# Performance work log

Hardware: AMD Instinct MI355X
Metric: run time of the kernel (lower is better)

Reference implementation:

```python
import jax, jax.numpy as jnp
import numpy as np

N, E = 50000, 800000
IN_DIM, NH = 256, 64          # in_dim, num_hidden
HID = 2 * NH                  # per-head out of GAT layers = num_hidden*2 = 128
HEADS, C = 2, 32              # heads[0]=heads[1]=2, final head=1, num_classes=32
NEG = 0.2                     # leaky relu negative slope


def _gat(h, W, al, ar, b, src, dst, heads, out, identity_res=False, res_W=None, act=None):
    # DGL-style GATConv: linear -> per-head attn logits -> edge softmax over dst -> scatter sum
    n = h.shape[0]
    feat = (h @ W).reshape(n, heads, out)              # [N, H, D]
    el = (feat * al).sum(-1)                           # [N, H]
    er = (feat * ar).sum(-1)                           # [N, H]
    e = el[src] + er[dst]                              # [E, H]
    e = jnp.where(e > 0, e, NEG * e)                   # leaky relu
    emax = jax.ops.segment_max(e, dst, num_segments=n)
    ex = jnp.exp(e - emax[dst])
    den = jax.ops.segment_sum(ex, dst, num_segments=n)
    alpha = ex / den[dst]                              # edge softmax per dst
    msg = feat[src] * alpha[..., None]                 # [E, H, D]
    rst = jax.ops.segment_sum(msg, dst, num_segments=n)  # [N, H, D]
    if identity_res:
        rst = rst + h.reshape(n, heads, out)
    elif res_W is not None:
        rst = rst + (h @ res_W).reshape(n, heads, out)
    rst = rst + b.reshape(1, heads, out)
    return act(rst) if act is not None else rst


def setup_inputs() -> dict:
    key = jax.random.key(0)
    ks = jax.random.split(key, 24)
    g = lambda i, shp, s: jax.random.normal(ks[i], shp, jnp.float32) * s
    d = {
        'inputs': g(0, (N, IN_DIM), 1.0),
        'z': g(1, (NH,), 1.0),
        'src': jax.random.randint(ks[2], (E,), 0, N, jnp.int32),
        'dst': jax.random.randint(ks[3], (E,), 0, N, jnp.int32),
        # x_to_h
        'Wx': g(4, (IN_DIM, NH), 0.06), 'bx': jnp.zeros((NH,), jnp.float32),
        # GAT layer 0: in 2*NH=128 -> heads=2, out=128
        'W0': g(5, (HID, HEADS * HID), 0.09), 'al0': g(6, (HEADS, HID), 0.09),
        'ar0': g(7, (HEADS, HID), 0.09), 'b0': jnp.zeros((HEADS * HID,), jnp.float32),
        # GAT layer 1: in 256 -> heads=2, out=128 (identity residual)
        'W1': g(8, (HEADS * HID, HEADS * HID), 0.06), 'al1': g(9, (HEADS, HID), 0.09),
        'ar1': g(10, (HEADS, HID), 0.09), 'b1': jnp.zeros((HEADS * HID,), jnp.float32),
        # final GAT: in 256 -> 1 head, out=num_classes=32, linear residual
        'Wf': g(11, (HEADS * HID, C), 0.06), 'alf': g(12, (1, C), 0.18),
        'arf': g(13, (1, C), 0.18), 'bf': jnp.zeros((C,), jnp.float32),
        'resWf': g(14, (HEADS * HID, C), 0.06),
    }
    return d


def reference(inputs, z, src, dst, Wx, bx, W0, al0, ar0, b0, W1, al1, ar1, b1, Wf, alf, arf, bf, resWf):
    n = inputs.shape[0]
    h = jax.nn.relu(inputs @ Wx + bx)                          # [N, NH]
    h = jnp.concatenate([h, jnp.broadcast_to(z, (n, z.shape[0]))], axis=1)  # [N, 2*NH]
    h = h / (jnp.linalg.norm(h, axis=1, keepdims=True) + 1e-6)
    h = _gat(h, W0, al0, ar0, b0, src, dst, HEADS, HID, act=jax.nn.elu).reshape(n, -1)
    h = _gat(h, W1, al1, ar1, b1, src, dst, HEADS, HID, identity_res=True, act=jax.nn.elu).reshape(n, -1)
    logits = _gat(h, Wf, alf, arf, bf, src, dst, 1, C, res_W=resWf).mean(1)  # [N, C]
    return logits
```

## Files before the change

### kernel.cpp

```cpp
#include <hip/hip_runtime.h>
#include <hip/hip_bf16.h>
#include <math.h>

#define N_NODES 50000
#define N_EDGES 800000
#define NEG 0.2f

typedef __attribute__((ext_vector_type(4))) float f32x4;
typedef __attribute__((ext_vector_type(8))) short bf16x8;

__device__ __forceinline__ float bf2f(ushort u) {
    union { uint i; float f; } t; t.i = ((uint)u) << 16; return t.f;
}
__device__ __forceinline__ ushort f2bf(float f) {
    union { float f; uint i; } t; t.f = f;
    uint i = t.i;
    uint r = (i + 0x7FFFu + ((i >> 16) & 1u)) >> 16;
    return (ushort)r;
}
__device__ __forceinline__ uint cvtpk(float lo, float hi) {
    uint r;
    asm("v_cvt_pk_bf16_f32 %0, %1, %2" : "=v"(r) : "v"(lo), "v"(hi));
    return r;
}

__device__ __forceinline__ void gload16(const ushort* src, ushort* ldst) {
    __builtin_amdgcn_global_load_lds(
        (const __attribute__((address_space(1))) uint32_t*)src,
        (__attribute__((address_space(3))) uint32_t*)ldst, 16, 0, 0);
}

__global__ void k_fillp(const int* __restrict__ src, const int* __restrict__ dst,
                        int* __restrict__ cnt, int* __restrict__ esrc, int E) {
    int e = blockIdx.x * 256 + threadIdx.x;
    if (e < E) {
        int d = dst[e];
        int p = atomicAdd(&cnt[d], 1);
        if (p < 64) esrc[((size_t)d << 6) + p] = src[e];
    }
}

__global__ void k_prep2(const float* __restrict__ Wx, const float* __restrict__ W0,
                        const float* __restrict__ W1, const float* __restrict__ Wf,
                        const float* __restrict__ rWf, const float* __restrict__ z,
                        ushort* __restrict__ BtX, ushort* __restrict__ Bt0,
                        ushort* __restrict__ Bt1, ushort* __restrict__ BtF,
                        float* __restrict__ zW0, int* __restrict__ cnt) {
    int i = blockIdx.x * 256 + threadIdx.x;
    const int base3 = 131072 + 256;
    if (i < 16384) {
        int n = i >> 8, k = i & 255;
        BtX[i] = f2bf(Wx[k * 64 + n]);
    } else if (i < 49152) {
        int t = i - 16384;
        int n = t >> 7, k = t & 127;
        Bt0[t] = f2bf(W0[k * 256 + n]);
    } else if (i < 114688) {
        int t = i - 49152;
        int n = t >> 8, k = t & 255;
        Bt1[t] = f2bf(W1[k * 256 + n]);
    } else if (i < 131072) {
        int t = i - 114688;
        int n = t >> 8, k = t & 255;
        float v = (n < 32) ? Wf[k * 32 + n] : rWf[k * 32 + (n - 32)];
        BtF[t] = f2bf(v);
    } else if (i < base3) {
        int c = i - 131072;
        float s = 0.f;
        for (int k = 0; k < 64; ++k) s += z[k] * W0[(64 + k) * 256 + c];
        zW0[c] = s;
    } else if (i < base3 + N_NODES) {
        cnt[i - base3] = 0;
    }
}

__global__ __launch_bounds__(256) void k_gemmA(
    const float* __restrict__ Ax, const ushort* __restrict__ BtX,
    const ushort* __restrict__ Bt0, const float* __restrict__ bx,
    const float* __restrict__ zv, const float* __restrict__ zW0,
    const float* __restrict__ alv, const float* __restrict__ arv,
    ushort* __restrict__ feat, float* __restrict__ elv, float* __restrict__ erv, int M)
{
    __shared__ ushort As1[128 * 64];
    __shared__ ushort Bs1[64 * 64];
    __shared__ ushort As2[128 * 64];
    __shared__ ushort Bs2[256 * 64];
    __shared__ float  invRow[128];

    const int tid = threadIdx.x;
    const int bm = blockIdx.x * 128;
    const int lane = tid & 63;
    const int w = tid >> 6;
    const int fr = lane & 15;
    const int kg = lane >> 4;
    const int rl = lane >> 3;
    const int bl = lane & 7;

    #pragma unroll
    for (int i = w; i < 32; i += 4) {
        int r = i * 8 + rl;
        int cb = bl ^ (r & 7);
        gload16(Bt0 + (size_t)r * 128 + cb * 8, &Bs2[i * 512]);
    }

    f32x4 acc1[2][4];
    #pragma unroll
    for (int m = 0; m < 2; ++m)
        #pragma unroll
        for (int n = 0; n < 4; ++n) acc1[m][n] = (f32x4){0.f, 0.f, 0.f, 0.f};

    const int ar_ = tid >> 1;
    const int ab_ = (tid & 1) * 4;
    int agr = bm + ar_; if (agr >= M) agr = 0;
    const float* ap0 = Ax + (size_t)agr * 256 + ab_ * 8;

    for (int k0 = 0; k0 < 256; k0 += 64) {
        {
            const float* ap = ap0 + k0;
            #pragma unroll
            for (int b = 0; b < 4; ++b) {
                float4 v0 = *(const float4*)(ap + b * 8);
                float4 v1 = *(const float4*)(ap + b * 8 + 4);
                uint4 pk;
                pk.x = cvtpk(v0.x, v0.y);
                pk.y = cvtpk(v0.z, v0.w);
                pk.z = cvtpk(v1.x, v1.y);
                pk.w = cvtpk(v1.z, v1.w);
                int p = (ab_ + b) ^ (ar_ & 7);
                *(uint4*)&As1[ar_ * 64 + p * 8] = pk;
            }
        }
        #pragma unroll
        for (int i = w; i < 8; i += 4) {
            int r = i * 8 + rl;
            int cb = bl ^ (r & 7);
            gload16(BtX + (size_t)r * 256 + k0 + cb * 8, &Bs1[i * 512]);
        }
        __syncthreads();
        #pragma unroll
        for (int s = 0; s < 2; ++s) {
            bf16x8 a[2], b[4];
            #pragma unroll
            for (int m = 0; m < 2; ++m) {
                int row = w * 32 + m * 16 + fr;
                int blk = (s * 4 + kg) ^ (fr & 7);
                a[m] = *(const bf16x8*)&As1[row * 64 + blk * 8];
            }
            #pragma unroll
            for (int n = 0; n < 4; ++n) {
                int row = n * 16 + fr;
                int blk = (s * 4 + kg) ^ (fr & 7);
                b[n] = *(const bf16x8*)&Bs1[row * 64 + blk * 8];
            }
            #pragma unroll
            for (int m = 0; m < 2; ++m)
                #pragma unroll
                for (int n = 0; n < 4; ++n)
                    acc1[m][n] = __builtin_amdgcn_mfma_f32_16x16x32_bf16(a[m], b[n], acc1[m][n], 0, 0, 0);
        }
        __syncthreads();
    }

    {
        float zl = zv[lane];
        float zq = zl * zl;
        #pragma unroll
        for (int off = 32; off > 0; off >>= 1) zq += __shfl_xor(zq, off, 64);
        #pragma unroll
        for (int m = 0; m < 2; ++m) {
            #pragma unroll
            for (int j = 0; j < 4; ++j) {
                int row = w * 32 + m * 16 + kg * 4 + j;
                float v[4]; float ss = 0.f;
                #pragma unroll
                for (int n = 0; n < 4; ++n) {
                    float o = acc1[m][n][j] + bx[n * 16 + fr];
                    o = fmaxf(o, 0.f);
                    v[n] = o; ss += o * o;
                }
                #pragma unroll
                for (int off = 8; off > 0; off >>= 1) ss += __shfl_xor(ss, off, 64);
                float inv = 1.f / (sqrtf(ss + zq) + 1e-6f);
                if (fr == 0) invRow[row] = inv;
                #pragma unroll
                for (int n = 0; n < 4; ++n) {
                    int b = n * 2 + (fr >> 3);
                    int p = b ^ (row & 7);
                    As2[row * 64 + p * 8 + (fr & 7)] = f2bf(v[n] * inv);
                }
            }
        }
    }
    __syncthreads();

    const int wr2 = w >> 1, wc2 = w & 1;
    f32x4 acc2[4][8];
    #pragma unroll
    for (int m = 0; m < 4; ++m)
        #pragma unroll
        for (int n = 0; n < 8; ++n) acc2[m][n] = (f32x4){0.f, 0.f, 0.f, 0.f};
    #pragma unroll
    for (int s = 0; s < 2; ++s) {
        bf16x8 a[4], b[8];
        #pragma unroll
        for (int m = 0; m < 4; ++m) {
            int row = wr2 * 64 + m * 16 + fr;
            int blk = (s * 4 + kg) ^ (fr & 7);
            a[m] = *(const bf16x8*)&As2[row * 64 + blk * 8];
        }
        #pragma unroll
        for (int n = 0; n < 8; ++n) {
            int row = wc2 * 128 + n * 16 + fr;
            int blk = (s * 4 + kg) ^ (fr & 7);
            b[n] = *(const bf16x8*)&Bs2[row * 64 + blk * 8];
        }
        #pragma unroll
        for (int m = 0; m < 4; ++m)
            #pragma unroll
            for (int n = 0; n < 8; ++n)
                acc2[m][n] = __builtin_amdgcn_mfma_f32_16x16x32_bf16(a[m], b[n], acc2[m][n], 0, 0, 0);
    }

    #pragma unroll
    for (int m = 0; m < 4; ++m) {
        #pragma unroll
        for (int j = 0; j < 4; ++j) {
            int lrow = wr2 * 64 + m * 16 + kg * 4 + j;
            int row = bm + lrow;
            float invR = invRow[lrow];
            float pe = 0.f, pr = 0.f;
            if (row < M) {
                #pragma unroll
                for (int n = 0; n < 8; ++n) {
                    int col = wc2 * 128 + n * 16 + fr;
                    float o = acc2[m][n][j] + invR * zW0[col];
                    feat[(size_t)row * 256 + col] = f2bf(o);
                    pe += o * alv[col];
                    pr += o * arv[col];
                }
            }
            #pragma unroll
            for (int off = 8; off > 0; off >>= 1) {
                pe += __shfl_xor(pe, off, 64);
                pr += __shfl_xor(pr, off, 64);
            }
            if (row < M && fr == 0) {
                elv[(size_t)row * 2 + wc2] = pe;
                erv[(size_t)row * 2 + wc2] = pr;
            }
        }
    }
}

__global__ __launch_bounds__(256) void k_gemmB(
    const ushort* __restrict__ A, const ushort* __restrict__ Bt,
    ushort* __restrict__ feat, const float* __restrict__ alv, const float* __restrict__ arv,
    float* __restrict__ elv, float* __restrict__ erv, int M)
{
    __shared__ ushort As[128 * 64];
    __shared__ ushort Bs[256 * 64];

    const int tid = threadIdx.x;
    const int bm = blockIdx.x * 128;
    const int lane = tid & 63;
    const int w = tid >> 6;
    const int wr = w >> 1, wc = w & 1;
    const int fr = lane & 15;
    const int kg = lane >> 4;
    const int rl = lane >> 3;
    const int bl = lane & 7;

    f32x4 acc[4][8];
    #pragma unroll
    for (int m = 0; m < 4; ++m)
        #pragma unroll
        for (int n = 0; n < 8; ++n) acc[m][n] = (f32x4){0.f, 0.f, 0.f, 0.f};

    for (int k0 = 0; k0 < 256; k0 += 64) {
        #pragma unroll
        for (int i = w; i < 16; i += 4) {
            int r = i * 8 + rl;
            int cb = bl ^ (r & 7);
            int gr = bm + r;
            if (gr >= M) gr = 0;
            gload16(A + (size_t)gr * 256 + k0 + cb * 8, &As[i * 512]);
        }
        #pragma unroll
        for (int i = w; i < 32; i += 4) {
            int r = i * 8 + rl;
            int cb = bl ^ (r & 7);
            gload16(Bt + (size_t)r * 256 + k0 + cb * 8, &Bs[i * 512]);
        }
        __syncthreads();
        #pragma unroll
        for (int s = 0; s < 2; ++s) {
            bf16x8 a[4], b[8];
            #pragma unroll
            for (int m = 0; m < 4; ++m) {
                int row = wr * 64 + m * 16 + fr;
                int blk = (s * 4 + kg) ^ (fr & 7);
                a[m] = *(const bf16x8*)&As[row * 64 + blk * 8];
            }
            #pragma unroll
            for (int n = 0; n < 8; ++n) {
                int row = wc * 128 + n * 16 + fr;
                int blk = (s * 4 + kg) ^ (fr & 7);
                b[n] = *(const bf16x8*)&Bs[row * 64 + blk * 8];
            }
            #pragma unroll
            for (int m = 0; m < 4; ++m)
                #pragma unroll
                for (int n = 0; n < 8; ++n)
                    acc[m][n] = __builtin_amdgcn_mfma_f32_16x16x32_bf16(a[m], b[n], acc[m][n], 0, 0, 0);
        }
        __syncthreads();
    }

    #pragma unroll
    for (int m = 0; m < 4; ++m) {
        #pragma unroll
        for (int j = 0; j < 4; ++j) {
            int row = bm + wr * 64 + m * 16 + kg * 4 + j;
            float pe = 0.f, pr = 0.f;
            if (row < M) {
                #pragma unroll
                for (int n = 0; n < 8; ++n) {
                    int col = wc * 128 + n * 16 + fr;
                    float o = acc[m][n][j];
                    feat[(size_t)row * 256 + col] = f2bf(o);
                    pe += o * alv[col];
                    pr += o * arv[col];
                }
            }
            #pragma unroll
            for (int off = 8; off > 0; off >>= 1) {
                pe += __shfl_xor(pe, off, 64);
                pr += __shfl_xor(pr, off, 64);
            }
            if (row < M && fr == 0) {
                elv[(size_t)row * 2 + wc] = pe;
                erv[(size_t)row * 2 + wc] = pr;
            }
        }
    }
}

__global__ __launch_bounds__(256) void k_gemmC(
    const ushort* __restrict__ A, const ushort* __restrict__ Bt,
    ushort* __restrict__ pkb, float* __restrict__ C2,
    const float* __restrict__ alv, const float* __restrict__ arv,
    float* __restrict__ elv, float* __restrict__ erv, int M)
{
    __shared__ ushort As[128 * 64];
    __shared__ ushort Bs[64 * 64];

    const int tid = threadIdx.x;
    const int bm = blockIdx.x * 128;
    const int lane = tid & 63;
    const int w = tid >> 6;
    const int fr = lane & 15;
    const int kg = lane >> 4;
    const int rl = lane >> 3;
    const int bl = lane & 7;

    f32x4 acc[2][4];
    #pragma unroll
    for (int m = 0; m < 2; ++m)
        #pragma unroll
        for (int n = 0; n < 4; ++n) acc[m][n] = (f32x4){0.f, 0.f, 0.f, 0.f};

    for (int k0 = 0; k0 < 256; k0 += 64) {
        #pragma unroll
        for (int i = w; i < 16; i += 4) {
            int r = i * 8 + rl;
            int cb = bl ^ (r & 7);
            int gr = bm + r;
            if (gr >= M) gr = 0;
            gload16(A + (size_t)gr * 256 + k0 + cb * 8, &As[i * 512]);
        }
        #pragma unroll
        for (int i = w; i < 8; i += 4) {
            int r = i * 8 + rl;
            int cb = bl ^ (r & 7);
            gload16(Bt + (size_t)r * 256 + k0 + cb * 8, &Bs[i * 512]);
        }
        __syncthreads();
        #pragma unroll
        for (int s = 0; s < 2; ++s) {
            bf16x8 a[2], b[4];
            #pragma unroll
            for (int m = 0; m < 2; ++m) {
                int row = w * 32 + m * 16 + fr;
                int blk = (s * 4 + kg) ^ (fr & 7);
                a[m] = *(const bf16x8*)&As[row * 64 + blk * 8];
            }
            #pragma unroll
            for (int n = 0; n < 4; ++n) {
                int row = n * 16 + fr;
                int blk = (s * 4 + kg) ^ (fr & 7);
                b[n] = *(const bf16x8*)&Bs[row * 64 + blk * 8];
            }
            #pragma unroll
            for (int m = 0; m < 2; ++m)
                #pragma unroll
                for (int n = 0; n < 4; ++n)
                    acc[m][n] = __builtin_amdgcn_mfma_f32_16x16x32_bf16(a[m], b[n], acc[m][n], 0, 0, 0);
        }
        __syncthreads();
    }

    #pragma unroll
    for (int m = 0; m < 2; ++m) {
        #pragma unroll
        for (int j = 0; j < 4; ++j) {
            int row = bm + w * 32 + m * 16 + kg * 4 + j;
            float pe = 0.f, pr = 0.f;
            if (row < M) {
                #pragma unroll
                for (int n = 0; n < 4; ++n) {
                    int col = n * 16 + fr;
                    float o = acc[m][n][j];
                    pkb[(size_t)row * 64 + col] = f2bf(o);
                    if (n >= 2) {
                        C2[(size_t)row * 32 + (col - 32)] = o;
                    } else {
                        pe += o * alv[col];
                        pr += o * arv[col];
                    }
                }
            }
            #pragma unroll
            for (int off = 8; off > 0; off >>= 1) {
                pe += __shfl_xor(pe, off, 64);
                pr += __shfl_xor(pr, off, 64);
            }
            if (row < M && fr == 0) { elv[row] = pe; erv[row] = pr; }
        }
    }
}

template<int RES>
__global__ __launch_bounds__(256) void k_edge256(
    const ushort* __restrict__ feat, const float* __restrict__ el, const float* __restrict__ er,
    const float* __restrict__ bias, const int* __restrict__ cnt, const int* __restrict__ esrc,
    ushort* __restrict__ outp, const ushort* __restrict__ resid, int n)
{
    __shared__ int2 swb[4][2][32];
    int wid = (blockIdx.x * blockDim.x + threadIdx.x) >> 6;
    int lane = threadIdx.x & 63;
    int w = threadIdx.x >> 6;
    if (wid >= n) return;
    int m = lane & 31;
    int head = lane >> 5;
    int deg = cnt[wid]; if (deg > 64) deg = 64;
    int rs = wid << 6, re = rs + deg;
    float ern = er[((size_t)wid << 1) + head];
    const char* featc = (const char*)feat;
    uint loff = (uint)lane << 3;

    float den[4] = {0.f, 0.f, 0.f, 0.f};
    f32x4 av[4];
    #pragma unroll
    for (int u = 0; u < 4; ++u) av[u] = (f32x4){0.f, 0.f, 0.f, 0.f};

    for (int c = rs; c < re; c += 32) {
        int nj = re - c; if (nj > 32) nj = 32;
        if (m < nj) {
            int s = esrc[c + m];
            float x = el[((uint)s << 1) + head] + ern;
            x = (x > 0.f) ? x : NEG * x;
            float wv = __expf(fminf(x, 60.f));
            int2 t; t.x = s; t.y = __float_as_int(wv);
            swb[w][head][m] = t;
        }
        int j = 0;
        for (; j + 3 < nj; j += 4) {
            #pragma unroll
            for (int u = 0; u < 4; ++u) {
                int2 p = swb[w][head][j + u];
                float wU = __int_as_float(p.y);
                ushort4 vU = *(const ushort4*)(featc + (((uint)p.x << 9) | loff));
                den[u] += wU;
                av[u].x += wU * bf2f(vU.x);
                av[u].y += wU * bf2f(vU.y);
                av[u].z += wU * bf2f(vU.z);
                av[u].w += wU * bf2f(vU.w);
            }
        }
        for (; j < nj; ++j) {
            int2 p = swb[w][head][j];
            float wU = __int_as_float(p.y);
            ushort4 vU = *(const ushort4*)(featc + (((uint)p.x << 9) | loff));
            den[0] += wU;
            av[0].x += wU * bf2f(vU.x);
            av[0].y += wU * bf2f(vU.y);
            av[0].z += wU * bf2f(vU.z);
            av[0].w += wU * bf2f(vU.w);
        }
    }
    float denT = (den[0] + den[1]) + (den[2] + den[3]);
    float ax = (av[0].x + av[1].x) + (av[2].x + av[3].x);
    float ay = (av[0].y + av[1].y) + (av[2].y + av[3].y);
    float az = (av[0].z + av[1].z) + (av[2].z + av[3].z);
    float aw = (av[0].w + av[1].w) + (av[2].w + av[3].w);
    float inv = (deg > 0) ? 1.f / denT : 0.f;

    int c0i = lane * 4;
    float4 bv = *(const float4*)(bias + c0i);
    float rx = 0.f, ry = 0.f, rz = 0.f, rw = 0.f;
    if (RES) {
        ushort4 rv = ((const ushort4*)resid)[(size_t)wid * 64 + lane];
        rx = bf2f(rv.x); ry = bf2f(rv.y); rz = bf2f(rv.z); rw = bf2f(rv.w);
    }
    float ox = ax * inv + bv.x + rx;
    float oy = ay * inv + bv.y + ry;
    float oz = az * inv + bv.z + rz;
    float ow = aw * inv + bv.w + rw;
    ox = (ox > 0.f) ? ox : expm1f(ox);
    oy = (oy > 0.f) ? oy : expm1f(oy);
    oz = (oz > 0.f) ? oz : expm1f(oz);
    ow = (ow > 0.f) ? ow : expm1f(ow);
    ushort4 o;
    o.x = f2bf(ox); o.y = f2bf(oy); o.z = f2bf(oz); o.w = f2bf(ow);
    ((ushort4*)outp)[(size_t)wid * 64 + lane] = o;
}

__global__ __launch_bounds__(256) void k_edgef(
    const ushort* __restrict__ pkb, const float* __restrict__ residf,
    const float* __restrict__ elf, const float* __restrict__ erf,
    const float* __restrict__ bfv, const int* __restrict__ cnt, const int* __restrict__ esrc,
    float* __restrict__ outp, int n)
{
    __shared__ int2 swf[16][16];
    int t = blockIdx.x * 256 + threadIdx.x;
    int node = t >> 4;
    int m = t & 15;
    int nb = threadIdx.x >> 4;
    if (node >= n) return;
    int deg = cnt[node]; if (deg > 64) deg = 64;
    int rs = node << 6, re = rs + deg;
    float ern = erf[node];
    const char* pc = (const char*)pkb;
    uint moff = (uint)m << 2;

    float den[4] = {0.f, 0.f, 0.f, 0.f};
    float a0[4] = {0.f, 0.f, 0.f, 0.f};
    float a1[4] = {0.f, 0.f, 0.f, 0.f};

    for (int c = rs; c < re; c += 16) {
        int nj = re - c; if (nj > 16) nj = 16;
        if (m < nj) {
            int s = esrc[c + m];
            float x = elf[s] + ern;
            x = (x > 0.f) ? x : NEG * x;
            float wv = __expf(fminf(x, 60.f));
            int2 tt; tt.x = s; tt.y = __float_as_int(wv);
            swf[nb][m] = tt;
        }
        int j = 0;
        for (; j + 3 < nj; j += 4) {
            #pragma unroll
            for (int u = 0; u < 4; ++u) {
                int2 p = swf[nb][j + u];
                float wU = __int_as_float(p.y);
                ushort2 vU = *(const ushort2*)(pc + (((uint)p.x << 7) | moff));
                den[u] += wU;
                a0[u] += wU * bf2f(vU.x);
                a1[u] += wU * bf2f(vU.y);
            }
        }
        for (; j < nj; ++j) {
            int2 p = swf[nb][j];
            float wU = __int_as_float(p.y);
            ushort2 vU = *(const ushort2*)(pc + (((uint)p.x << 7) | moff));
            den[0] += wU;
            a0[0] += wU * bf2f(vU.x);
            a1[0] += wU * bf2f(vU.y);
        }
    }
    float dT = (den[0] + den[1]) + (den[2] + den[3]);
    float A0 = (a0[0] + a0[1]) + (a0[2] + a0[3]);
    float A1 = (a1[0] + a1[1]) + (a1[2] + a1[3]);
    float inv = (deg > 0) ? 1.f / dT : 0.f;

    float2 rv = *(const float2*)(residf + (size_t)node * 32 + 2 * m);
    float2 bv = *(const float2*)(bfv + 2 * m);
    float2 o;
    o.x = A0 * inv + rv.x + bv.x;
    o.y = A1 * inv + rv.y + bv.y;
    *(float2*)(outp + (size_t)node * 32 + 2 * m) = o;
}

extern "C" void kernel_launch(void* const* d_in, const int* in_sizes, int n_in,
                              void* d_out, int out_size, void* d_ws, size_t ws_size,
                              hipStream_t stream) {
    const float* inputs = (const float*)d_in[0];
    const float* z      = (const float*)d_in[1];
    const int*   src    = (const int*)d_in[2];
    const int*   dst    = (const int*)d_in[3];
    const float* Wx  = (const float*)d_in[4];
    const float* bx  = (const float*)d_in[5];
    const float* W0  = (const float*)d_in[6];
    const float* al0 = (const float*)d_in[7];
    const float* ar0 = (const float*)d_in[8];
    const float* b0  = (const float*)d_in[9];
    const float* W1  = (const float*)d_in[10];
    const float* al1 = (const float*)d_in[11];
    const float* ar1 = (const float*)d_in[12];
    const float* b1  = (const float*)d_in[13];
    const float* Wf  = (const float*)d_in[14];
    const float* alf = (const float*)d_in[15];
    const float* arf = (const float*)d_in[16];
    const float* bf  = (const float*)d_in[17];
    const float* rWf = (const float*)d_in[18];
    float* out = (float*)d_out;

    const int N = N_NODES, E = N_EDGES;

    char* w = (char*)d_ws;
    auto alloc = [&](size_t bytes) -> char* {
        char* p = w;
        w += (bytes + 255) & ~(size_t)255;
        return p;
    };
    ushort* feat  = (ushort*)alloc((size_t)N * 256 * 2);
    ushort* h1    = (ushort*)alloc((size_t)N * 256 * 2);
    ushort* h2    = (ushort*)alloc((size_t)N * 256 * 2);
    ushort* pkb   = (ushort*)alloc((size_t)N * 64 * 2);
    float*  residf= (float*)alloc((size_t)N * 32 * 4);
    float*  elerb = (float*)alloc((size_t)N * 4 * 4);
    float*  elb   = elerb;
    float*  erb   = elerb + (size_t)N * 2;
    ushort* BtX   = (ushort*)alloc((size_t)64 * 256 * 2);
    ushort* Bt0   = (ushort*)alloc((size_t)256 * 128 * 2);
    ushort* Bt1   = (ushort*)alloc((size_t)256 * 256 * 2);
    ushort* BtF   = (ushort*)alloc((size_t)64 * 256 * 2);
    float*  zW0   = (float*)alloc(256 * 4);
    int* cnt  = (int*)alloc((size_t)N * 4);
    int* esrc = (int*)alloc((size_t)N * 64 * 4);

    int prep_threads = 131072 + 256 + N;
    k_prep2<<<(prep_threads + 255) / 256, 256, 0, stream>>>(Wx, W0, W1, Wf, rWf, z,
                                                            BtX, Bt0, Bt1, BtF, zW0, cnt);
    k_fillp<<<(E + 255) / 256, 256, 0, stream>>>(src, dst, cnt, esrc, E);

    int nwb = (N + 3) / 4;
    int ngb = (N + 127) / 128;

    k_gemmA<<<ngb, 256, 0, stream>>>(inputs, BtX, Bt0, bx, z, zW0, al0, ar0, feat, elb, erb, N);
    k_edge256<0><<<nwb, 256, 0, stream>>>(feat, elb, erb, b0, cnt, esrc, h1, nullptr, N);

    k_gemmB<<<ngb, 256, 0, stream>>>(h1, Bt1, feat, al1, ar1, elb, erb, N);
    k_edge256<1><<<nwb, 256, 0, stream>>>(feat, elb, erb, b1, cnt, esrc, h2, h1, N);

    k_gemmC<<<ngb, 256, 0, stream>>>(h2, BtF, pkb, residf, alf, arf, elb, erb, N);
    k_edgef<<<(N + 15) / 16, 256, 0, stream>>>(pkb, residf, elb, erb, bf, cnt, esrc, out, N);
}
```

Before: 265.2 us.

## Widen gather loads in edge aggregation kernels and split edges across half-waves

The two edge-aggregation kernels now have each lane load wider vectors of bf16 features (16 bytes instead of 8 in the 256-wide kernel, 8 instead of 4 in the final kernel). The two halves of the lane group handle alternating edges, and their partial sums are combined with a cross-lane shuffle before the epilogue, which only half the lanes execute. The aim is fewer, wider global load instructions and more edges in flight per instruction on the random-gather path. In exchange, each lane holds more accumulator registers, the tail loop loads a dummy row (node 0) with weight zero, and half the lanes sit idle during the output write.

```diff
diff --git a/kernel.cpp b/kernel.cpp
--- a/kernel.cpp
+++ b/kernel.cpp
@@ -451,78 +451,106 @@
     int w = threadIdx.x >> 6;
     if (wid >= n) return;
     int m = lane & 31;
-    int head = lane >> 5;
+    int headw = lane >> 5;
+    int q = lane >> 5;
+    int h = lane & 31;
+    int headc = h >> 4;
     int deg = cnt[wid]; if (deg > 64) deg = 64;
     int rs = wid << 6, re = rs + deg;
-    float ern = er[((size_t)wid << 1) + head];
+    float ern = er[((size_t)wid << 1) + headw];
     const char* featc = (const char*)feat;
-    uint loff = (uint)lane << 3;
-
-    float den[4] = {0.f, 0.f, 0.f, 0.f};
-    f32x4 av[4];
-    #pragma unroll
-    for (int u = 0; u < 4; ++u) av[u] = (f32x4){0.f, 0.f, 0.f, 0.f};
+    uint loff = (uint)h << 4;
+
+    float den[2] = {0.f, 0.f};
+    float ac[2][8];
+    #pragma unroll
+    for (int u = 0; u < 2; ++u)
+        #pragma unroll
+        for (int k = 0; k < 8; ++k) ac[u][k] = 0.f;
 
     for (int c = rs; c < re; c += 32) {
         int nj = re - c; if (nj > 32) nj = 32;
         if (m < nj) {
             int s = esrc[c + m];
-            float x = el[((uint)s << 1) + head] + ern;
+            float x = el[((uint)s << 1) + headw] + ern;
             x = (x > 0.f) ? x : NEG * x;
             float wv = __expf(fminf(x, 60.f));
             int2 t; t.x = s; t.y = __float_as_int(wv);
-            swb[w][head][m] = t;
+            swb[w][headw][m] = t;
         }
         int j = 0;
-        for (; j + 3 < nj; j += 4) {
+        for (; j + 7 < nj; j += 8) {
             #pragma unroll
             for (int u = 0; u < 4; ++u) {
-                int2 p = swb[w][head][j + u];
+                int e = j + 2 * u + q;
+                int2 p = swb[w][headc][e];
                 float wU = __int_as_float(p.y);
-                ushort4 vU = *(const ushort4*)(featc + (((uint)p.x << 9) | loff));
-                den[u] += wU;
-                av[u].x += wU * bf2f(vU.x);
-                av[u].y += wU * bf2f(vU.y);
-                av[u].z += wU * bf2f(vU.z);
-                av[u].w += wU * bf2f(vU.w);
-            }
-        }
-        for (; j < nj; ++j) {
-            int2 p = swb[w][head][j];
-            float wU = __int_as_float(p.y);
-            ushort4 vU = *(const ushort4*)(featc + (((uint)p.x << 9) | loff));
+                uint4 vU = *(const uint4*)(featc + (((uint)p.x << 9) | loff));
+                den[u & 1] += wU;
+                ac[u & 1][0] += wU * __int_as_float(vU.x << 16);
+                ac[u & 1][1] += wU * __int_as_float(vU.x & 0xffff0000u);
+                ac[u & 1][2] += wU * __int_as_float(vU.y << 16);
+                ac[u & 1][3] += wU * __int_as_float(vU.y & 0xffff0000u);
+                ac[u & 1][4] += wU * __int_as_float(vU.z << 16);
+                ac[u & 1][5] += wU * __int_as_float(vU.z & 0xffff0000u);
+                ac[u & 1][6] += wU * __int_as_float(vU.w << 16);
+                ac[u & 1][7] += wU * __int_as_float(vU.w & 0xffff0000u);
+            }
+        }
+        for (; j < nj; j += 2) {
+            int e = j + q;
+            int sU = 0; float wU = 0.f;
+            if (e < nj) {
+                int2 p = swb[w][headc][e];
+                sU = p.x; wU = __int_as_float(p.y);
+            }
+            uint4 vU = *(const uint4*)(featc + (((uint)sU << 9) | loff));
             den[0] += wU;
-            av[0].x += wU * bf2f(vU.x);
-            av[0].y += wU * bf2f(vU.y);
-            av[0].z += wU * bf2f(vU.z);
-            av[0].w += wU * bf2f(vU.w);
-        }
-    }
-    float denT = (den[0] + den[1]) + (den[2] + den[3]);
-    float ax = (av[0].x + av[1].x) + (av[2].x + av[3].x);
-    float ay = (av[0].y + av[1].y) + (av[2].y + av[3].y);
-    float az = (av[0].z + av[1].z) + (av[2].z + av[3].z);
-    float aw = (av[0].w + av[1].w) + (av[2].w + av[3].w);
-    float inv = (deg > 0) ? 1.f / denT : 0.f;
-
-    int c0i = lane * 4;
-    float4 bv = *(const float4*)(bias + c0i);
-    float rx = 0.f, ry = 0.f, rz = 0.f, rw = 0.f;
-    if (RES) {
-        ushort4 rv = ((const ushort4*)resid)[(size_t)wid * 64 + lane];
-        rx = bf2f(rv.x); ry = bf2f(rv.y); rz = bf2f(rv.z); rw = bf2f(rv.w);
-    }
-    float ox = ax * inv + bv.x + rx;
-    float oy = ay * inv + bv.y + ry;
-    float oz = az * inv + bv.z + rz;
-    float ow = aw * inv + bv.w + rw;
-    ox = (ox > 0.f) ? ox : expm1f(ox);
-    oy = (oy > 0.f) ? oy : expm1f(oy);
-    oz = (oz > 0.f) ? oz : expm1f(oz);
-    ow = (ow > 0.f) ? ow : expm1f(ow);
-    ushort4 o;
-    o.x = f2bf(ox); o.y = f2bf(oy); o.z = f2bf(oz); o.w = f2bf(ow);
-    ((ushort4*)outp)[(size_t)wid * 64 + lane] = o;
+            ac[0][0] += wU * __int_as_float(vU.x << 16);
+            ac[0][1] += wU * __int_as_float(vU.x & 0xffff0000u);
+            ac[0][2] += wU * __int_as_float(vU.y << 16);
+            ac[0][3] += wU * __int_as_float(vU.y & 0xffff0000u);
+            ac[0][4] += wU * __int_as_float(vU.z << 16);
+            ac[0][5] += wU * __int_as_float(vU.z & 0xffff0000u);
+            ac[0][6] += wU * __int_as_float(vU.w << 16);
+            ac[0][7] += wU * __int_as_float(vU.w & 0xffff0000u);
+        }
+    }
+
+    float dT = den[0] + den[1];
+    dT += __shfl_xor(dT, 32, 64);
+    float at[8];
+    #pragma unroll
+    for (int k = 0; k < 8; ++k) {
+        at[k] = ac[0][k] + ac[1][k];
+        at[k] += __shfl_xor(at[k], 32, 64);
+    }
+    float inv = (deg > 0) ? 1.f / dT : 0.f;
+
+    if (lane < 32) {
+        float bv[8];
+        *(float4*)&bv[0] = *(const float4*)(bias + h * 8);
+        *(float4*)&bv[4] = *(const float4*)(bias + h * 8 + 4);
+        float rv[8] = {0.f, 0.f, 0.f, 0.f, 0.f, 0.f, 0.f, 0.f};
+        if (RES) {
+            uint4 rr = ((const uint4*)resid)[(size_t)wid * 32 + h];
+            rv[0] = __int_as_float(rr.x << 16); rv[1] = __int_as_float(rr.x & 0xffff0000u);
+            rv[2] = __int_as_float(rr.y << 16); rv[3] = __int_as_float(rr.y & 0xffff0000u);
+            rv[4] = __int_as_float(rr.z << 16); rv[5] = __int_as_float(rr.z & 0xffff0000u);
+            rv[6] = __int_as_float(rr.w << 16); rv[7] = __int_as_float(rr.w & 0xffff0000u);
+        }
+        uint ou[4];
+        #pragma unroll
+        for (int k2 = 0; k2 < 4; ++k2) {
+            float o0 = at[2 * k2]     * inv + bv[2 * k2]     + rv[2 * k2];
+            float o1 = at[2 * k2 + 1] * inv + bv[2 * k2 + 1] + rv[2 * k2 + 1];
+            o0 = (o0 > 0.f) ? o0 : expm1f(o0);
+            o1 = (o1 > 0.f) ? o1 : expm1f(o1);
+            ou[k2] = (uint)f2bf(o0) | ((uint)f2bf(o1) << 16);
+        }
+        uint4 ov; ov.x = ou[0]; ov.y = ou[1]; ov.z = ou[2]; ov.w = ou[3];
+        ((uint4*)outp)[(size_t)wid * 32 + h] = ov;
+    }
 }
 
 __global__ __launch_bounds__(256) void k_edgef(
@@ -537,15 +565,20 @@
     int m = t & 15;
     int nb = threadIdx.x >> 4;
     if (node >= n) return;
+    int q = m >> 3;
+    int h = m & 7;
     int deg = cnt[node]; if (deg > 64) deg = 64;
     int rs = node << 6, re = rs + deg;
     float ern = erf[node];
     const char* pc = (const char*)pkb;
-    uint moff = (uint)m << 2;
-
-    float den[4] = {0.f, 0.f, 0.f, 0.f};
-    float a0[4] = {0.f, 0.f, 0.f, 0.f};
-    float a1[4] = {0.f, 0.f, 0.f, 0.f};
+    uint moff = (uint)h << 3;
+
+    float den[2] = {0.f, 0.f};
+    float ac[2][4];
+    #pragma unroll
+    for (int u = 0; u < 2; ++u)
+        #pragma unroll
+        for (int k = 0; k < 4; ++k) ac[u][k] = 0.f;
 
     for (int c = rs; c < re; c += 16) {
         int nj = re - c; if (nj > 16) nj = 16;
@@ -558,37 +591,56 @@
             swf[nb][m] = tt;
         }
         int j = 0;
-        for (; j + 3 < nj; j += 4) {
+        for (; j + 7 < nj; j += 8) {
             #pragma unroll
             for (int u = 0; u < 4; ++u) {
-                int2 p = swf[nb][j + u];
+                int e = j + 2 * u + q;
+                int2 p = swf[nb][e];
                 float wU = __int_as_float(p.y);
-                ushort2 vU = *(const ushort2*)(pc + (((uint)p.x << 7) | moff));
-                den[u] += wU;
-                a0[u] += wU * bf2f(vU.x);
-                a1[u] += wU * bf2f(vU.y);
-            }
-        }
-        for (; j < nj; ++j) {
-            int2 p = swf[nb][j];
-            float wU = __int_as_float(p.y);
-            ushort2 vU = *(const ushort2*)(pc + (((uint)p.x << 7) | moff));
+                uint2 vU = *(const uint2*)(pc + (((uint)p.x << 7) | moff));
+                den[u & 1] += wU;
+                ac[u & 1][0] += wU * __int_as_float(vU.x << 16);
+                ac[u & 1][1] += wU * __int_as_float(vU.x & 0xffff0000u);
+                ac[u & 1][2] += wU * __int_as_float(vU.y << 16);
+                ac[u & 1][3] += wU * __int_as_float(vU.y & 0xffff0000u);
+            }
+        }
+        for (; j < nj; j += 2) {
+            int e = j + q;
+            int sU = 0; float wU = 0.f;
+            if (e < nj) {
+                int2 p = swf[nb][e];
+                sU = p.x; wU = __int_as_float(p.y);
+            }
+            uint2 vU = *(const uint2*)(pc + (((uint)sU << 7) | moff));
             den[0] += wU;
-            a0[0] += wU * bf2f(vU.x);
-            a1[0] += wU * bf2f(vU.y);
-        }
-    }
-    float dT = (den[0] + den[1]) + (den[2] + den[3]);
-    float A0 = (a0[0] + a0[1]) + (a0[2] + a0[3]);
-    float A1 = (a1[0] + a1[1]) + (a1[2] + a1[3]);
+            ac[0][0] += wU * __int_as_float(vU.x << 16);
+            ac[0][1] += wU * __int_as_float(vU.x & 0xffff0000u);
+            ac[0][2] += wU * __int_as_float(vU.y << 16);
+            ac[0][3] += wU * __int_as_float(vU.y & 0xffff0000u);
+        }
+    }
+
+    float dT = den[0] + den[1];
+    dT += __shfl_xor(dT, 8, 16);
+    float at[4];
+    #pragma unroll
+    for (int k = 0; k < 4; ++k) {
+        at[k] = ac[0][k] + ac[1][k];
+        at[k] += __shfl_xor(at[k], 8, 16);
+    }
     float inv = (deg > 0) ? 1.f / dT : 0.f;
 
-    float2 rv = *(const float2*)(residf + (size_t)node * 32 + 2 * m);
-    float2 bv = *(const float2*)(bfv + 2 * m);
-    float2 o;
-    o.x = A0 * inv + rv.x + bv.x;
-    o.y = A1 * inv + rv.y + bv.y;
-    *(float2*)(outp + (size_t)node * 32 + 2 * m) = o;
+    if (m < 8) {
+        float4 rv = *(const float4*)(residf + (size_t)node * 32 + 4 * h);
+        float4 bv = *(const float4*)(bfv + 4 * h);
+        float4 o;
+        o.x = at[0] * inv + rv.x + bv.x;
+        o.y = at[1] * inv + rv.y + bv.y;
+        o.z = at[2] * inv + rv.z + bv.z;
+        o.w = at[3] * inv + rv.w + bv.w;
+        *(float4*)(outp + (size_t)node * 32 + 4 * h) = o;
+    }
 }
 
 extern "C" void kernel_launch(void* const* d_in, const int* in_sizes, int n_in,
```

Result: no change. 269.7 us (+1.7%).
